# Kernel tuning notes

Measured on AMD Instinct MI355X. Metric: run time of the kernel, lower is better.

## Reference

```python
import jax, jax.numpy as jnp
import numpy as np

N_EMB = 1024
N_HEAD = 16
HEAD_DIM = N_EMB // N_HEAD


def setup_inputs() -> dict:
    key = jax.random.key(0)
    k_x, k_wa, k_ba, k_wp, k_bp = jax.random.split(key, 5)
    B, S = 4, 2048
    scale = 1.0 / np.sqrt(N_EMB)
    return {
        "x": jax.random.normal(k_x, (B, S, N_EMB), dtype=jnp.float32),
        "W_attn": jax.random.normal(k_wa, (N_EMB, 3 * N_EMB), dtype=jnp.float32) * scale,
        "b_attn": jax.random.normal(k_ba, (3 * N_EMB,), dtype=jnp.float32) * 0.01,
        "W_proj": jax.random.normal(k_wp, (N_EMB, N_EMB), dtype=jnp.float32) * scale,
        "b_proj": jax.random.normal(k_bp, (N_EMB,), dtype=jnp.float32) * 0.01,
    }


def _attention(x, W_attn, b_attn, W_proj, b_proj):
    B, S, E = x.shape
    qkv = x @ W_attn + b_attn  # [B, S, 3E]
    q, k, v = jnp.split(qkv, 3, axis=-1)
    # [B, H, S, D]
    q = q.reshape(B, S, N_HEAD, HEAD_DIM).transpose(0, 2, 1, 3)
    k = k.reshape(B, S, N_HEAD, HEAD_DIM).transpose(0, 2, 1, 3)
    v = v.reshape(B, S, N_HEAD, HEAD_DIM).transpose(0, 2, 1, 3)
    scores = jnp.einsum("bhqd,bhkd->bhqk", q, k) / jnp.sqrt(jnp.asarray(HEAD_DIM, x.dtype))
    causal = jnp.tril(jnp.ones((S, S), dtype=bool))
    scores = jnp.where(causal, scores, jnp.asarray(-jnp.inf, x.dtype))
    probs = jax.nn.softmax(scores, axis=-1)
    y = jnp.einsum("bhqk,bhkd->bhqd", probs, v)  # [B, H, S, D]
    y = y.transpose(0, 2, 1, 3).reshape(B, S, E)
    return y @ W_proj + b_proj


def reference(x, W_attn, b_attn, W_proj, b_proj):
    return _attention(x, W_attn, b_attn, W_proj, b_proj)
```

## Files before the change

kernel.cpp:

```cpp
#include <hip/hip_runtime.h>
#include <hip/hip_bf16.h>

typedef __bf16 bf16x8 __attribute__((ext_vector_type(8)));
typedef __bf16 bf16x4 __attribute__((ext_vector_type(4)));
typedef float f32x4 __attribute__((ext_vector_type(4)));

#define MFMA16(a, b, c) __builtin_amdgcn_mfma_f32_16x16x32_bf16(a, b, c, 0, 0, 0)

#define BATCH 4
#define SEQ   2048
#define EMB   1024
#define NHEAD 16
#define HDIM  64
#define ROWS  (BATCH * SEQ)
#define N_QKV (3 * EMB)
#define BH_STRIDE (SEQ * HDIM)

__device__ __forceinline__ void gload_lds16(const __bf16* gp, __bf16* lp) {
  __builtin_amdgcn_global_load_lds(
      (const __attribute__((address_space(1))) void*)gp,
      (__attribute__((address_space(3))) void*)lp, 16, 0, 0);
}

__global__ void cast_f32_to_bf16_x4(const float* __restrict__ src,
                                    __bf16* __restrict__ dst, int n4) {
  int i = blockIdx.x * blockDim.x + threadIdx.x;
  if (i >= n4) return;
  float4 f = ((const float4*)src)[i];
  bf16x4 o;
  o.x = (__bf16)f.x; o.y = (__bf16)f.y; o.z = (__bf16)f.z; o.w = (__bf16)f.w;
  ((bf16x4*)dst)[i] = o;
}

__global__ void transpose_to_bf16(const float* __restrict__ src,
                                  __bf16* __restrict__ dst, int R, int C) {
  __shared__ float t[32][33];
  int c0 = blockIdx.x * 32, r0 = blockIdx.y * 32;
  int tx = threadIdx.x, ty = threadIdx.y;
#pragma unroll
  for (int i = 0; i < 32; i += 8)
    t[ty + i][tx] = src[(size_t)(r0 + ty + i) * C + c0 + tx];
  __syncthreads();
#pragma unroll
  for (int i = 0; i < 32; i += 8)
    dst[(size_t)(c0 + ty + i) * R + r0 + tx] = (__bf16)t[tx][ty + i];
}

__global__ __launch_bounds__(256) void gemm_qkv(
    const __bf16* __restrict__ A, const __bf16* __restrict__ Bt,
    const float* __restrict__ bias,
    __bf16* __restrict__ Qt, __bf16* __restrict__ Kt, __bf16* __restrict__ Vt) {
  const int K = EMB;
  __shared__ __align__(16) __bf16 sA[128 * 32];
  __shared__ __align__(16) __bf16 sB[128 * 32];
  int id = blockIdx.x;
  int xcd = id & 7, j5 = id >> 3;
  int by = j5 >> 3;
  int bx = xcd * 8 + (j5 & 7);
  int m0 = by * 128, n0 = bx * 128;
  int tid = threadIdx.x;
  int wave = tid >> 6, lane = tid & 63;
  int wr = wave >> 1, wc = wave & 1;
  int l16 = lane & 15, quad = lane >> 4, quad4 = quad * 4;
  int f1 = tid * 8;
  int r1 = f1 >> 5, c1 = f1 & 31;
  int f2 = f1 + 2048;
  int r2 = f2 >> 5, c2 = f2 & 31;
  f32x4 acc[4][4] = {};
  for (int k0 = 0; k0 < K; k0 += 32) {
    gload_lds16(A + (size_t)(m0 + r1) * K + k0 + c1, &sA[wave * 512]);
    gload_lds16(A + (size_t)(m0 + r2) * K + k0 + c2, &sA[2048 + wave * 512]);
    gload_lds16(Bt + (size_t)(n0 + r1) * K + k0 + c1, &sB[wave * 512]);
    gload_lds16(Bt + (size_t)(n0 + r2) * K + k0 + c2, &sB[2048 + wave * 512]);
    __syncthreads();
    bf16x8 a[4], b[4];
#pragma unroll
    for (int i = 0; i < 4; i++)
      a[i] = *(const bf16x8*)(sA + (wr * 64 + i * 16 + l16) * 32 + quad * 8);
#pragma unroll
    for (int j = 0; j < 4; j++)
      b[j] = *(const bf16x8*)(sB + (wc * 64 + j * 16 + l16) * 32 + quad * 8);
#pragma unroll
    for (int i = 0; i < 4; i++)
#pragma unroll
      for (int j = 0; j < 4; j++) acc[i][j] = MFMA16(a[i], b[j], acc[i][j]);
    __syncthreads();
  }
  const float KSC = 0.18033688011112043f;
  int sec = m0 >> 10;
#pragma unroll
  for (int i = 0; i < 4; i++) {
    int e0 = m0 + wr * 64 + i * 16 + quad4;
    float4 bv4 = *(const float4*)(bias + e0);
    int h = (e0 & 1023) >> 6, d0 = e0 & 63;
#pragma unroll
    for (int j = 0; j < 4; j++) {
      int scol = n0 + wc * 64 + j * 16 + l16;
      int bidx = scol >> 11, s = scol & 2047;
      size_t base = (size_t)(bidx * NHEAD + h) * BH_STRIDE;
      float v0 = acc[i][j][0] + bv4.x;
      float v1 = acc[i][j][1] + bv4.y;
      float v2 = acc[i][j][2] + bv4.z;
      float v3 = acc[i][j][3] + bv4.w;
      if (sec == 0) {
        int idx = (s >> 4) * 1024 + (d0 >> 5) * 512 + ((d0 >> 3) & 3) * 128 +
                  (s & 15) * 8 + (d0 & 7);
        bf16x4 o4;
        o4.x = (__bf16)(v0 * KSC); o4.y = (__bf16)(v1 * KSC);
        o4.z = (__bf16)(v2 * KSC); o4.w = (__bf16)(v3 * KSC);
        *(bf16x4*)(Qt + base + idx) = o4;
      } else if (sec == 1) {
        int idx = (s >> 6) * 4096 + ((s >> 4) & 3) * 1024 + (d0 >> 5) * 512 +
                  ((d0 >> 3) & 3) * 128 + (s & 15) * 8 + (d0 & 7);
        bf16x4 o4;
        o4.x = (__bf16)v0; o4.y = (__bf16)v1;
        o4.z = (__bf16)v2; o4.w = (__bf16)v3;
        *(bf16x4*)(Kt + base + idx) = o4;
      } else {
        int idx = (s >> 6) * 4096 + (d0 >> 4) * 1024 + ((s >> 5) & 1) * 512 +
                  ((s >> 2) & 3) * 128 + ((s >> 4) & 1) * 4 + (s & 3) +
                  quad4 * 8;
        Vt[base + idx] = (__bf16)v0;
        Vt[base + idx + 8] = (__bf16)v1;
        Vt[base + idx + 16] = (__bf16)v2;
        Vt[base + idx + 24] = (__bf16)v3;
      }
    }
  }
}

__global__ __launch_bounds__(256, 4) void attn_fwd(
    const __bf16* __restrict__ Qt, const __bf16* __restrict__ Kt,
    const __bf16* __restrict__ Vt, __bf16* __restrict__ Y) {
  __shared__ __align__(16) __bf16 sK[2][4096];
  __shared__ __align__(16) __bf16 sV[2][4096];
  int id = blockIdx.x;
  int g = id >> 6;
  int qb = 15 - g;
  int hb = id & 63;
  int h = hb >> 2, b = hb & 3;
  int tid = threadIdx.x;
  int wave = tid >> 6, lane = tid & 63;
  int l16 = lane & 15, quad = lane >> 4, quad4 = quad * 4;
  int q0 = qb * 128;
  size_t bh = (size_t)b * NHEAD + h;
  const __bf16* Qh = Qt + bh * BH_STRIDE;
  const __bf16* Kh = Kt + bh * BH_STRIDE;
  const __bf16* Vh = Vt + bh * BH_STRIDE;
  int mq = q0 + wave * 32;
  const __bf16* qbase = Qh + (size_t)(mq >> 4) * 1024 + lane * 8;
  bf16x8 qa0 = *(const bf16x8*)(qbase);
  bf16x8 qa1 = *(const bf16x8*)(qbase + 512);
  bf16x8 qb0 = *(const bf16x8*)(qbase + 1024);
  bf16x8 qb1 = *(const bf16x8*)(qbase + 1536);
  f32x4 accA[4] = {}, accB[4] = {};
  float lA = 0.f, lB = 0.f;
  const float NEG_INF = -__builtin_inff();
  int nt = (q0 + 128) >> 6;
  gload_lds16(Kh + tid * 8, sK[0] + tid * 8);
  gload_lds16(Kh + 2048 + tid * 8, sK[0] + 2048 + tid * 8);
  gload_lds16(Vh + tid * 8, sV[0] + tid * 8);
  gload_lds16(Vh + 2048 + tid * 8, sV[0] + 2048 + tid * 8);
  __syncthreads();
  int cur = 0;
  for (int it = 0; it < nt; ++it) {
    int kt = it * 64;
    if (it + 1 < nt) {
      const __bf16* kg = Kh + (size_t)(it + 1) * 4096 + tid * 8;
      const __bf16* vg = Vh + (size_t)(it + 1) * 4096 + tid * 8;
      __bf16* dK = sK[cur ^ 1] + tid * 8;
      __bf16* dV = sV[cur ^ 1] + tid * 8;
      gload_lds16(kg, dK);
      gload_lds16(kg + 2048, dK + 2048);
      gload_lds16(vg, dV);
      gload_lds16(vg + 2048, dV + 2048);
    }
    if (kt <= mq + 31) {
      const __bf16* sKc = sK[cur];
      const __bf16* sVc = sV[cur];
      bool diag = (kt + 64 > mq);
      int relA = mq + l16 - kt;
      int relB = relA + 16;
      bf16x8 PA0, PA1, PB0, PB1;
      __builtin_amdgcn_s_setprio(1);
#pragma unroll
      for (int t = 0; t < 4; t++) {
        bf16x8 ka = *(const bf16x8*)(sKc + t * 1024 + lane * 8);
        bf16x8 kb = *(const bf16x8*)(sKc + t * 1024 + 512 + lane * 8);
        f32x4 zA = {}, zB = {};
        zA = MFMA16(ka, qa0, zA);
        zA = MFMA16(kb, qa1, zA);
        zB = MFMA16(ka, qb0, zB);
        zB = MFMA16(kb, qb1, zB);
        int kl = t * 16 + quad4;
        float pA[4], pB[4];
        if (diag) {
#pragma unroll
          for (int r = 0; r < 4; r++) {
            pA[r] = __builtin_amdgcn_exp2f(kl + r > relA ? NEG_INF : zA[r]);
            pB[r] = __builtin_amdgcn_exp2f(kl + r > relB ? NEG_INF : zB[r]);
          }
        } else {
#pragma unroll
          for (int r = 0; r < 4; r++) {
            pA[r] = __builtin_amdgcn_exp2f(zA[r]);
            pB[r] = __builtin_amdgcn_exp2f(zB[r]);
          }
        }
        lA += (pA[0] + pA[1]) + (pA[2] + pA[3]);
        lB += (pB[0] + pB[1]) + (pB[2] + pB[3]);
        if (t == 0) {
          PA0[0] = (__bf16)pA[0]; PA0[1] = (__bf16)pA[1];
          PA0[2] = (__bf16)pA[2]; PA0[3] = (__bf16)pA[3];
          PB0[0] = (__bf16)pB[0]; PB0[1] = (__bf16)pB[1];
          PB0[2] = (__bf16)pB[2]; PB0[3] = (__bf16)pB[3];
        } else if (t == 1) {
          PA0[4] = (__bf16)pA[0]; PA0[5] = (__bf16)pA[1];
          PA0[6] = (__bf16)pA[2]; PA0[7] = (__bf16)pA[3];
          PB0[4] = (__bf16)pB[0]; PB0[5] = (__bf16)pB[1];
          PB0[6] = (__bf16)pB[2]; PB0[7] = (__bf16)pB[3];
        } else if (t == 2) {
          PA1[0] = (__bf16)pA[0]; PA1[1] = (__bf16)pA[1];
          PA1[2] = (__bf16)pA[2]; PA1[3] = (__bf16)pA[3];
          PB1[0] = (__bf16)pB[0]; PB1[1] = (__bf16)pB[1];
          PB1[2] = (__bf16)pB[2]; PB1[3] = (__bf16)pB[3];
        } else {
          PA1[4] = (__bf16)pA[0]; PA1[5] = (__bf16)pA[1];
          PA1[6] = (__bf16)pA[2]; PA1[7] = (__bf16)pA[3];
          PB1[4] = (__bf16)pB[0]; PB1[5] = (__bf16)pB[1];
          PB1[6] = (__bf16)pB[2]; PB1[7] = (__bf16)pB[3];
        }
      }
#pragma unroll
      for (int jj = 0; jj < 4; jj++) {
        bf16x8 va = *(const bf16x8*)(sVc + jj * 1024 + lane * 8);
        bf16x8 vb = *(const bf16x8*)(sVc + jj * 1024 + 512 + lane * 8);
        accA[jj] = MFMA16(va, PA0, accA[jj]);
        accA[jj] = MFMA16(vb, PA1, accA[jj]);
        accB[jj] = MFMA16(va, PB0, accB[jj]);
        accB[jj] = MFMA16(vb, PB1, accB[jj]);
      }
      __builtin_amdgcn_s_setprio(0);
    }
    __syncthreads();
    cur ^= 1;
  }
  lA += __shfl_xor(lA, 16); lA += __shfl_xor(lA, 32);
  lB += __shfl_xor(lB, 16); lB += __shfl_xor(lB, 32);
  float invA = 1.f / lA, invB = 1.f / lB;
  int gqA = mq + l16, gqB = mq + 16 + l16;
#pragma unroll
  for (int jj = 0; jj < 4; jj++) {
    bf16x4 oA, oB;
    oA.x = (__bf16)(accA[jj][0] * invA);
    oA.y = (__bf16)(accA[jj][1] * invA);
    oA.z = (__bf16)(accA[jj][2] * invA);
    oA.w = (__bf16)(accA[jj][3] * invA);
    oB.x = (__bf16)(accB[jj][0] * invB);
    oB.y = (__bf16)(accB[jj][1] * invB);
    oB.z = (__bf16)(accB[jj][2] * invB);
    oB.w = (__bf16)(accB[jj][3] * invB);
    *(bf16x4*)(Y + ((size_t)b * SEQ + gqA) * EMB + h * HDIM + jj * 16 + quad4) = oA;
    *(bf16x4*)(Y + ((size_t)b * SEQ + gqB) * EMB + h * HDIM + jj * 16 + quad4) = oB;
  }
}

__global__ __launch_bounds__(256) void gemm_proj(
    const __bf16* __restrict__ A, const __bf16* __restrict__ Bt,
    const float* __restrict__ bias, float* __restrict__ out) {
  const int K = EMB;
  __shared__ __align__(16) __bf16 sA[128 * 32];
  __shared__ __align__(16) __bf16 sB[128 * 32];
  int id = blockIdx.x;
  int lid = (id & 7) * (512 >> 3) + (id >> 3);
  int bx = lid & 7, by = lid >> 3;
  int m0 = by * 128, n0 = bx * 128;
  int tid = threadIdx.x;
  int wave = tid >> 6, lane = tid & 63;
  int wr = wave >> 1, wc = wave & 1;
  int l16 = lane & 15, quad = lane >> 4;
  int f1 = tid * 8;
  int r1 = f1 >> 5, c1 = f1 & 31;
  int f2 = f1 + 2048;
  int r2 = f2 >> 5, c2 = f2 & 31;
  f32x4 acc[4][4] = {};
  for (int k0 = 0; k0 < K; k0 += 32) {
    gload_lds16(A + (size_t)(m0 + r1) * K + k0 + c1, &sA[wave * 512]);
    gload_lds16(A + (size_t)(m0 + r2) * K + k0 + c2, &sA[2048 + wave * 512]);
    gload_lds16(Bt + (size_t)(n0 + r1) * K + k0 + c1, &sB[wave * 512]);
    gload_lds16(Bt + (size_t)(n0 + r2) * K + k0 + c2, &sB[2048 + wave * 512]);
    __syncthreads();
    bf16x8 a[4], b[4];
#pragma unroll
    for (int i = 0; i < 4; i++)
      a[i] = *(const bf16x8*)(sA + (wr * 64 + i * 16 + l16) * 32 + quad * 8);
#pragma unroll
    for (int j = 0; j < 4; j++)
      b[j] = *(const bf16x8*)(sB + (wc * 64 + j * 16 + l16) * 32 + quad * 8);
#pragma unroll
    for (int i = 0; i < 4; i++)
#pragma unroll
      for (int j = 0; j < 4; j++) acc[i][j] = MFMA16(a[i], b[j], acc[i][j]);
    __syncthreads();
  }
#pragma unroll
  for (int i = 0; i < 4; i++) {
    int row = m0 + wr * 64 + i * 16 + quad * 4;
#pragma unroll
    for (int j = 0; j < 4; j++) {
      int col = n0 + wc * 64 + j * 16 + l16;
      float bv = bias[col];
#pragma unroll
      for (int r = 0; r < 4; r++)
        out[(size_t)(row + r) * EMB + col] = acc[i][j][r] + bv;
    }
  }
}

extern "C" void kernel_launch(void* const* d_in, const int* in_sizes, int n_in,
                              void* d_out, int out_size, void* d_ws, size_t ws_size,
                              hipStream_t stream) {
  const float* x      = (const float*)d_in[0];
  const float* W_attn = (const float*)d_in[1];
  const float* b_attn = (const float*)d_in[2];
  const float* W_proj = (const float*)d_in[3];
  const float* b_proj = (const float*)d_in[4];
  float* out = (float*)d_out;

  char* ws = (char*)d_ws;
  size_t off = 0;
  __bf16* xb   = (__bf16*)(ws + off); off += (size_t)ROWS * EMB * 2;
  __bf16* Wa_t = (__bf16*)(ws + off); off += (size_t)N_QKV * EMB * 2;
  __bf16* Wp_t = (__bf16*)(ws + off); off += (size_t)EMB * EMB * 2;
  __bf16* Qt   = (__bf16*)(ws + off); off += (size_t)ROWS * EMB * 2;
  __bf16* Kt   = (__bf16*)(ws + off); off += (size_t)ROWS * EMB * 2;
  __bf16* Vt   = (__bf16*)(ws + off); off += (size_t)ROWS * EMB * 2;
  __bf16* Yb   = (__bf16*)(ws + off); off += (size_t)ROWS * EMB * 2;

  {
    int n4 = ROWS * EMB / 4;
    cast_f32_to_bf16_x4<<<(n4 + 255) / 256, 256, 0, stream>>>(x, xb, n4);
    dim3 blk(32, 8);
    transpose_to_bf16<<<dim3(N_QKV / 32, EMB / 32), blk, 0, stream>>>(W_attn, Wa_t, EMB, N_QKV);
    transpose_to_bf16<<<dim3(EMB / 32, EMB / 32), blk, 0, stream>>>(W_proj, Wp_t, EMB, EMB);
  }
  gemm_qkv<<<dim3(1536), 256, 0, stream>>>(Wa_t, xb, b_attn, Qt, Kt, Vt);
  attn_fwd<<<dim3((SEQ / 128) * NHEAD * BATCH), 256, 0, stream>>>(Qt, Kt, Vt, Yb);
  gemm_proj<<<dim3(512), 256, 0, stream>>>(Yb, Wp_t, b_proj, out);
}
```

Before: 240.8 us.

## Fuse prep kernels and deepen GEMM K-tile to 64 with XOR-swizzled LDS

Merges the x cast and the two weight transposes into one launch that dispatches on block index, removing two kernel launches. Both GEMMs now stage a K-tile of 64 instead of 32 per barrier pair, halving the number of synchronizations, and use an XOR swizzle on the LDS column chunk to avoid bank conflicts on the fragment reads. This doubles shared memory per block, which may reduce occupancy.

```diff
diff --git a/kernel.cpp b/kernel.cpp
--- a/kernel.cpp
+++ b/kernel.cpp
@@ -22,28 +22,41 @@
       (__attribute__((address_space(3))) void*)lp, 16, 0, 0);
 }
 
-__global__ void cast_f32_to_bf16_x4(const float* __restrict__ src,
-                                    __bf16* __restrict__ dst, int n4) {
-  int i = blockIdx.x * blockDim.x + threadIdx.x;
-  if (i >= n4) return;
-  float4 f = ((const float4*)src)[i];
-  bf16x4 o;
-  o.x = (__bf16)f.x; o.y = (__bf16)f.y; o.z = (__bf16)f.z; o.w = (__bf16)f.w;
-  ((bf16x4*)dst)[i] = o;
-}
-
-__global__ void transpose_to_bf16(const float* __restrict__ src,
-                                  __bf16* __restrict__ dst, int R, int C) {
-  __shared__ float t[32][33];
-  int c0 = blockIdx.x * 32, r0 = blockIdx.y * 32;
-  int tx = threadIdx.x, ty = threadIdx.y;
+__global__ void prep_fused(const float* __restrict__ x,
+                           const float* __restrict__ W_attn,
+                           const float* __restrict__ W_proj,
+                           __bf16* __restrict__ xb,
+                           __bf16* __restrict__ Wa_t,
+                           __bf16* __restrict__ Wp_t) {
+  __shared__ float tt[32][33];
+  int bid = blockIdx.x, tid = threadIdx.x;
+  if (bid < 8192) {
+    int i = bid * 256 + tid;
+    float4 f = ((const float4*)x)[i];
+    bf16x4 o;
+    o.x = (__bf16)f.x; o.y = (__bf16)f.y; o.z = (__bf16)f.z; o.w = (__bf16)f.w;
+    ((bf16x4*)xb)[i] = o;
+    return;
+  }
+  const float* src; __bf16* dst; int R, C, bx, by;
+  if (bid < 8192 + 3072) {
+    int t = bid - 8192;
+    src = W_attn; dst = Wa_t; R = EMB; C = N_QKV;
+    bx = t % 96; by = t / 96;
+  } else {
+    int t = bid - 11264;
+    src = W_proj; dst = Wp_t; R = EMB; C = EMB;
+    bx = t & 31; by = t >> 5;
+  }
+  int c0 = bx * 32, r0 = by * 32;
+  int tx = tid & 31, ty = tid >> 5;
 #pragma unroll
   for (int i = 0; i < 32; i += 8)
-    t[ty + i][tx] = src[(size_t)(r0 + ty + i) * C + c0 + tx];
+    tt[ty + i][tx] = src[(size_t)(r0 + ty + i) * C + c0 + tx];
   __syncthreads();
 #pragma unroll
   for (int i = 0; i < 32; i += 8)
-    dst[(size_t)(c0 + ty + i) * R + r0 + tx] = (__bf16)t[tx][ty + i];
+    dst[(size_t)(c0 + ty + i) * R + r0 + tx] = (__bf16)tt[tx][ty + i];
 }
 
 __global__ __launch_bounds__(256) void gemm_qkv(
@@ -51,8 +64,8 @@
     const float* __restrict__ bias,
     __bf16* __restrict__ Qt, __bf16* __restrict__ Kt, __bf16* __restrict__ Vt) {
   const int K = EMB;
-  __shared__ __align__(16) __bf16 sA[128 * 32];
-  __shared__ __align__(16) __bf16 sB[128 * 32];
+  __shared__ __align__(16) __bf16 sA[128 * 64];
+  __shared__ __align__(16) __bf16 sB[128 * 64];
   int id = blockIdx.x;
   int xcd = id & 7, j5 = id >> 3;
   int by = j5 >> 3;
@@ -62,28 +75,36 @@
   int wave = tid >> 6, lane = tid & 63;
   int wr = wave >> 1, wc = wave & 1;
   int l16 = lane & 15, quad = lane >> 4, quad4 = quad * 4;
-  int f1 = tid * 8;
-  int r1 = f1 >> 5, c1 = f1 & 31;
-  int f2 = f1 + 2048;
-  int r2 = f2 >> 5, c2 = f2 & 31;
+  int l7 = l16 & 7;
+  int srow = tid >> 3;
+  int scol = ((tid & 7) ^ (srow & 7)) * 8;
   f32x4 acc[4][4] = {};
-  for (int k0 = 0; k0 < K; k0 += 32) {
-    gload_lds16(A + (size_t)(m0 + r1) * K + k0 + c1, &sA[wave * 512]);
-    gload_lds16(A + (size_t)(m0 + r2) * K + k0 + c2, &sA[2048 + wave * 512]);
-    gload_lds16(Bt + (size_t)(n0 + r1) * K + k0 + c1, &sB[wave * 512]);
-    gload_lds16(Bt + (size_t)(n0 + r2) * K + k0 + c2, &sB[2048 + wave * 512]);
-    __syncthreads();
-    bf16x8 a[4], b[4];
-#pragma unroll
-    for (int i = 0; i < 4; i++)
-      a[i] = *(const bf16x8*)(sA + (wr * 64 + i * 16 + l16) * 32 + quad * 8);
-#pragma unroll
-    for (int j = 0; j < 4; j++)
-      b[j] = *(const bf16x8*)(sB + (wc * 64 + j * 16 + l16) * 32 + quad * 8);
-#pragma unroll
-    for (int i = 0; i < 4; i++)
-#pragma unroll
-      for (int j = 0; j < 4; j++) acc[i][j] = MFMA16(a[i], b[j], acc[i][j]);
+  for (int k0 = 0; k0 < K; k0 += 64) {
+#pragma unroll
+    for (int q = 0; q < 4; q++)
+      gload_lds16(A + (size_t)(m0 + q * 32 + srow) * K + k0 + scol,
+                  &sA[q * 2048 + wave * 512]);
+#pragma unroll
+    for (int q = 0; q < 4; q++)
+      gload_lds16(Bt + (size_t)(n0 + q * 32 + srow) * K + k0 + scol,
+                  &sB[q * 2048 + wave * 512]);
+    __syncthreads();
+#pragma unroll
+    for (int kk = 0; kk < 2; kk++) {
+      bf16x8 a[4], b[4];
+#pragma unroll
+      for (int i = 0; i < 4; i++)
+        a[i] = *(const bf16x8*)(sA + (wr * 64 + i * 16 + l16) * 64 +
+                                (((kk * 4 + quad) ^ l7) * 8));
+#pragma unroll
+      for (int j = 0; j < 4; j++)
+        b[j] = *(const bf16x8*)(sB + (wc * 64 + j * 16 + l16) * 64 +
+                                (((kk * 4 + quad) ^ l7) * 8));
+#pragma unroll
+      for (int i = 0; i < 4; i++)
+#pragma unroll
+        for (int j = 0; j < 4; j++) acc[i][j] = MFMA16(a[i], b[j], acc[i][j]);
+    }
     __syncthreads();
   }
   const float KSC = 0.18033688011112043f;
@@ -95,8 +116,8 @@
     int h = (e0 & 1023) >> 6, d0 = e0 & 63;
 #pragma unroll
     for (int j = 0; j < 4; j++) {
-      int scol = n0 + wc * 64 + j * 16 + l16;
-      int bidx = scol >> 11, s = scol & 2047;
+      int scolv = n0 + wc * 64 + j * 16 + l16;
+      int bidx = scolv >> 11, s = scolv & 2047;
       size_t base = (size_t)(bidx * NHEAD + h) * BH_STRIDE;
       float v0 = acc[i][j][0] + bv4.x;
       float v1 = acc[i][j][1] + bv4.y;
@@ -269,8 +290,8 @@
     const __bf16* __restrict__ A, const __bf16* __restrict__ Bt,
     const float* __restrict__ bias, float* __restrict__ out) {
   const int K = EMB;
-  __shared__ __align__(16) __bf16 sA[128 * 32];
-  __shared__ __align__(16) __bf16 sB[128 * 32];
+  __shared__ __align__(16) __bf16 sA[128 * 64];
+  __shared__ __align__(16) __bf16 sB[128 * 64];
   int id = blockIdx.x;
   int lid = (id & 7) * (512 >> 3) + (id >> 3);
   int bx = lid & 7, by = lid >> 3;
@@ -279,28 +300,36 @@
   int wave = tid >> 6, lane = tid & 63;
   int wr = wave >> 1, wc = wave & 1;
   int l16 = lane & 15, quad = lane >> 4;
-  int f1 = tid * 8;
-  int r1 = f1 >> 5, c1 = f1 & 31;
-  int f2 = f1 + 2048;
-  int r2 = f2 >> 5, c2 = f2 & 31;
+  int l7 = l16 & 7;
+  int srow = tid >> 3;
+  int scol = ((tid & 7) ^ (srow & 7)) * 8;
   f32x4 acc[4][4] = {};
-  for (int k0 = 0; k0 < K; k0 += 32) {
-    gload_lds16(A + (size_t)(m0 + r1) * K + k0 + c1, &sA[wave * 512]);
-    gload_lds16(A + (size_t)(m0 + r2) * K + k0 + c2, &sA[2048 + wave * 512]);
-    gload_lds16(Bt + (size_t)(n0 + r1) * K + k0 + c1, &sB[wave * 512]);
-    gload_lds16(Bt + (size_t)(n0 + r2) * K + k0 + c2, &sB[2048 + wave * 512]);
-    __syncthreads();
-    bf16x8 a[4], b[4];
-#pragma unroll
-    for (int i = 0; i < 4; i++)
-      a[i] = *(const bf16x8*)(sA + (wr * 64 + i * 16 + l16) * 32 + quad * 8);
-#pragma unroll
-    for (int j = 0; j < 4; j++)
-      b[j] = *(const bf16x8*)(sB + (wc * 64 + j * 16 + l16) * 32 + quad * 8);
-#pragma unroll
-    for (int i = 0; i < 4; i++)
-#pragma unroll
-      for (int j = 0; j < 4; j++) acc[i][j] = MFMA16(a[i], b[j], acc[i][j]);
+  for (int k0 = 0; k0 < K; k0 += 64) {
+#pragma unroll
+    for (int q = 0; q < 4; q++)
+      gload_lds16(A + (size_t)(m0 + q * 32 + srow) * K + k0 + scol,
+                  &sA[q * 2048 + wave * 512]);
+#pragma unroll
+    for (int q = 0; q < 4; q++)
+      gload_lds16(Bt + (size_t)(n0 + q * 32 + srow) * K + k0 + scol,
+                  &sB[q * 2048 + wave * 512]);
+    __syncthreads();
+#pragma unroll
+    for (int kk = 0; kk < 2; kk++) {
+      bf16x8 a[4], b[4];
+#pragma unroll
+      for (int i = 0; i < 4; i++)
+        a[i] = *(const bf16x8*)(sA + (wr * 64 + i * 16 + l16) * 64 +
+                                (((kk * 4 + quad) ^ l7) * 8));
+#pragma unroll
+      for (int j = 0; j < 4; j++)
+        b[j] = *(const bf16x8*)(sB + (wc * 64 + j * 16 + l16) * 64 +
+                                (((kk * 4 + quad) ^ l7) * 8));
+#pragma unroll
+      for (int i = 0; i < 4; i++)
+#pragma unroll
+        for (int j = 0; j < 4; j++) acc[i][j] = MFMA16(a[i], b[j], acc[i][j]);
+    }
     __syncthreads();
   }
 #pragma unroll
@@ -337,13 +366,7 @@
   __bf16* Vt   = (__bf16*)(ws + off); off += (size_t)ROWS * EMB * 2;
   __bf16* Yb   = (__bf16*)(ws + off); off += (size_t)ROWS * EMB * 2;
 
-  {
-    int n4 = ROWS * EMB / 4;
-    cast_f32_to_bf16_x4<<<(n4 + 255) / 256, 256, 0, stream>>>(x, xb, n4);
-    dim3 blk(32, 8);
-    transpose_to_bf16<<<dim3(N_QKV / 32, EMB / 32), blk, 0, stream>>>(W_attn, Wa_t, EMB, N_QKV);
-    transpose_to_bf16<<<dim3(EMB / 32, EMB / 32), blk, 0, stream>>>(W_proj, Wp_t, EMB, EMB);
-  }
+  prep_fused<<<dim3(12288), 256, 0, stream>>>(x, W_attn, W_proj, xb, Wa_t, Wp_t);
   gemm_qkv<<<dim3(1536), 256, 0, stream>>>(Wa_t, xb, b_attn, Qt, Kt, Vt);
   attn_fwd<<<dim3((SEQ / 128) * NHEAD * BATCH), 256, 0, stream>>>(Qt, Kt, Vt, Yb);
   gemm_proj<<<dim3(512), 256, 0, stream>>>(Yb, Wp_t, b_proj, out);
```

Result: faster. 230.6 us (-4.2%).
